# Optimization experiments

Measured on AMD Instinct MI355X. Metric: run time of the kernel, lower is better.

Reference implementation:

```python
import jax, jax.numpy as jnp
import numpy as np

# ---- constants from FlyingCartpole.__init__ defaults ----
MASS_Q = 2.0
MASS_P = 0.1
MASS = MASS_Q + MASS_P              # total mass m
JMAT = jnp.array([[0.0023, 0.0, 0.0], [0.0, 0.0023, 0.0], [0.0, 0.0, 0.004]], jnp.float32)
JINV = jnp.linalg.inv(JMAT)
L = 0.5                              # pendulum length
GVEC = jnp.array([0.0, 0.0, -9.81], jnp.float32)
MOTOR_DIST = 0.175
KF = 1.0
KM = 0.025
DT = 0.05
ACT_SCALE = 10.0
U_HOVER = -MASS * (-9.81) / ACT_SCALE / KF / 4.0   # per-motor hover throttle
_SS = np.array([[1.0, 1, 0], [1.0, -1, 0], [-1.0, -1, 0], [-1.0, 1, 0]], np.float32)
SS = jnp.asarray(_SS / np.linalg.norm(_SS, axis=-1, keepdims=True))  # [4,3] unit arms


def mrp2quat(m):
    # q = [1 - |m|^2, 2m] / (1 + |m|^2)
    n2 = jnp.sum(m * m, axis=-1, keepdims=True)
    return jnp.concatenate([1.0 - n2, 2.0 * m], axis=-1) / (1.0 + n2)


def quatrot(q, v):
    # rotate vector v by unit quaternion q = [s, qv]
    s, qv = q[..., :1], q[..., 1:]
    return v + 2.0 * jnp.cross(qv, jnp.cross(qv, v) + s * v)


def w2pdotkinematics_mrp(m, w):
    # mdot = 1/4 [(1-|m|^2) I + 2 [m]_x + 2 m m^T] w
    n2 = jnp.sum(m * m, axis=-1, keepdims=True)
    mw = jnp.sum(m * w, axis=-1, keepdims=True)
    return 0.25 * ((1.0 - n2) * w + 2.0 * jnp.cross(m, w) + 2.0 * m * mw)


def dynamics_(x, u):
    # state: [r(3), m(3), theta(1), v(3), w(3), theta_dot(1)]
    u = ACT_SCALE * (u + U_HOVER)
    m = x[..., 3:6]
    v = x[..., 7:10]
    w = x[..., 10:13]
    theta = x[..., 6:7]
    theta_dot = x[..., 13:14]

    q = mrp2quat(m)

    # forces (body frame): thrust + gravity rotated by q(-m)
    Fz = KF * jnp.sum(u, axis=-1)                     # [B]
    z = jnp.zeros_like(Fz)
    Fvec = jnp.stack([z, z, Fz], axis=-1)             # [B,3]
    f = Fvec + quatrot(mrp2quat(-m), MASS * GVEC)     # [B,3]

    # moments
    tau3 = KM * (u[..., 0] - u[..., 1] + u[..., 2] - u[..., 3])
    tau = jnp.stack([z, z, tau3], axis=-1)            # [B,3]
    zu = jnp.zeros_like(u)
    thrust = jnp.stack([zu, zu, KF * u], axis=-1)     # [B,4,3]
    tau = tau + jnp.cross(MOTOR_DIST * SS, thrust).sum(axis=-2)

    mdot = w2pdotkinematics_mrp(m, w)
    pdot = quatrot(q, v)
    vdot = f / MASS - jnp.cross(w, v)
    Jw = jnp.einsum('ij,bj->bi', JMAT, w)
    wdot = jnp.einsum('ij,bj->bi', JINV, tau - jnp.cross(w, Jw))

    x_ddot = quatrot(q, vdot)[..., 0:1]
    theta_ddot = (GVEC[2] * jnp.sin(theta) + x_ddot * jnp.cos(theta)) / L
    return jnp.concatenate([pdot, mdot, theta_dot, vdot, wdot, theta_ddot], axis=-1)


def rk4_dynamics(x, u):
    dt, dt2 = DT, DT / 2.0
    k1 = dynamics_(x, u)
    k2 = dynamics_(x + dt2 * k1, u)
    k3 = dynamics_(x + dt2 * k2, u)
    k4 = dynamics_(x + dt * k3, u)
    return x + dt / 6.0 * (k1 + 2.0 * k2 + 2.0 * k3 + k4)


def setup_inputs() -> dict:
    key = jax.random.key(0)
    kx, ku = jax.random.split(key)
    B = 2097152
    x = jax.random.normal(kx, (B, 14), dtype=jnp.float32)
    u = jax.random.normal(ku, (B, 4), dtype=jnp.float32)
    return {"x": x, "u": u}


def reference(x, u):
    return rk4_dynamics(x, u)
```

## Files before the change

kernel.cpp:

```cpp
#include <hip/hip_runtime.h>
#include <math.h>

namespace fc {

typedef float vf2 __attribute__((ext_vector_type(2)));
typedef float vf4 __attribute__((ext_vector_type(4)));

__device__ __forceinline__ vf2 sp(float c) { return vf2{c, c}; }

constexpr float ACT_SCALE = 10.0f;
constexpr float U_HOVER   = 0.515025f;
constexpr float INV_MASS  = 1.0f / 2.1f;
constexpr float KM        = 0.025f;
constexpr float TAUC      = 0.175f * 0.70710678f;
constexpr float JXY       = 0.0023f;
constexpr float JZ        = 0.004f;
constexpr float INV_JXY   = 1.0f / 0.0023f;
constexpr float INV_JZ    = 1.0f / 0.004f;
constexpr float G3        = -9.81f;
constexpr float INV_L     = 2.0f;
constexpr float DT        = 0.05f;
constexpr float DT2       = 0.05f * 0.5f;
constexpr float DT6       = 0.05f / 6.0f;

__device__ __forceinline__ void dyn2(const vf2* xt, vf2 FzM,
                                     vf2 taux, vf2 tauy, vf2 tauz, vf2* dx) {
  vf2 mx = xt[3], my = xt[4], mz = xt[5], th = xt[6];
  vf2 vx = xt[7], vy = xt[8], vz = xt[9];
  vf2 wx = xt[10], wy = xt[11], wz = xt[12];

  vf2 n2 = mx * mx + my * my + mz * mz;
  vf2 inv;
  inv.x = __builtin_amdgcn_rcpf(1.0f + n2.x);
  inv.y = __builtin_amdgcn_rcpf(1.0f + n2.y);
  vf2 s  = (sp(1.0f) - n2) * inv;
  vf2 qx = sp(2.0f) * mx * inv;
  vf2 qy = sp(2.0f) * my * inv;
  vf2 qz = sp(2.0f) * mz * inv;

  vf2 gtx = qy * sp(-G3);
  vf2 gty = qx * sp(G3);
  vf2 gtz = s * sp(G3);
  vf2 gx = sp(-2.0f) * (qy * gtz - qz * gty);
  vf2 gy = sp(-2.0f) * (qz * gtx - qx * gtz);
  vf2 gz = sp(G3) + sp(-2.0f) * (qx * gty - qy * gtx);

  vf2 tx = qy * vz - qz * vy + s * vx;
  vf2 ty = qz * vx - qx * vz + s * vy;
  vf2 tz = qx * vy - qy * vx + s * vz;
  dx[0] = vx + sp(2.0f) * (qy * tz - qz * ty);
  dx[1] = vy + sp(2.0f) * (qz * tx - qx * tz);
  dx[2] = vz + sp(2.0f) * (qx * ty - qy * tx);

  vf2 mw  = mx * wx + my * wy + mz * wz;
  vf2 on2 = sp(1.0f) - n2;
  dx[3] = sp(0.25f) * (on2 * wx + sp(2.0f) * (my * wz - mz * wy) + sp(2.0f) * mx * mw);
  dx[4] = sp(0.25f) * (on2 * wy + sp(2.0f) * (mz * wx - mx * wz) + sp(2.0f) * my * mw);
  dx[5] = sp(0.25f) * (on2 * wz + sp(2.0f) * (mx * wy - my * wx) + sp(2.0f) * mz * mw);

  dx[6] = xt[13];

  vf2 vdx = gx - (wy * vz - wz * vy);
  vf2 vdy = gy - (wz * vx - wx * vz);
  vf2 vdz = FzM + gz - (wx * vy - wy * vx);
  dx[7] = vdx; dx[8] = vdy; dx[9] = vdz;

  vf2 Jwx = sp(JXY) * wx, Jwy = sp(JXY) * wy, Jwz = sp(JZ) * wz;
  dx[10] = (taux - (wy * Jwz - wz * Jwy)) * sp(INV_JXY);
  dx[11] = (tauy - (wz * Jwx - wx * Jwz)) * sp(INV_JXY);
  dx[12] = (tauz - (wx * Jwy - wy * Jwx)) * sp(INV_JZ);

  vf2 t2y = qz * vdx - qx * vdz + s * vdy;
  vf2 t2z = qx * vdy - qy * vdx + s * vdz;
  vf2 rx  = vdx + sp(2.0f) * (qy * t2z - qz * t2y);
  vf2 st, ct;
  st.x = __sinf(th.x); st.y = __sinf(th.y);
  ct.x = __cosf(th.x); ct.y = __cosf(th.y);
  dx[13] = (sp(G3) * st + rx * ct) * sp(INV_L);
}

__device__ __forceinline__ void rk4_rows2(const vf2* x0, vf4 uA, vf4 uB, vf2* o) {
  vf2 su0 = sp(ACT_SCALE) * (vf2{uA.x, uB.x} + sp(U_HOVER));
  vf2 su1 = sp(ACT_SCALE) * (vf2{uA.y, uB.y} + sp(U_HOVER));
  vf2 su2 = sp(ACT_SCALE) * (vf2{uA.z, uB.z} + sp(U_HOVER));
  vf2 su3 = sp(ACT_SCALE) * (vf2{uA.w, uB.w} + sp(U_HOVER));

  vf2 Fz   = ((su0 + su1) + su2) + su3;
  vf2 FzM  = Fz * sp(INV_MASS);
  vf2 tauz = sp(KM) * (((su0 - su1) + su2) - su3);
  vf2 taux = ((sp(TAUC) * su0 + sp(-TAUC) * su1) + sp(-TAUC) * su2) + sp(TAUC) * su3;
  vf2 tauy = ((sp(-TAUC) * su0 + sp(-TAUC) * su1) + sp(TAUC) * su2) + sp(TAUC) * su3;

  vf2 xt[14], kk[14], acc[14];
  dyn2(x0, FzM, taux, tauy, tauz, kk);
  #pragma unroll
  for (int j = 0; j < 14; ++j) { acc[j] = kk[j]; xt[j] = x0[j] + sp(DT2) * kk[j]; }
  dyn2(xt, FzM, taux, tauy, tauz, kk);
  #pragma unroll
  for (int j = 0; j < 14; ++j) { acc[j] += sp(2.0f) * kk[j]; xt[j] = x0[j] + sp(DT2) * kk[j]; }
  dyn2(xt, FzM, taux, tauy, tauz, kk);
  #pragma unroll
  for (int j = 0; j < 14; ++j) { acc[j] += sp(2.0f) * kk[j]; xt[j] = x0[j] + sp(DT) * kk[j]; }
  dyn2(xt, FzM, taux, tauy, tauz, kk);
  #pragma unroll
  for (int j = 0; j < 14; ++j) o[j] = x0[j] + sp(DT6) * (acc[j] + kk[j]);
}

__global__ __launch_bounds__(256) void fc_rk4_kernel(const float* __restrict__ x,
                                                     const float* __restrict__ u,
                                                     float* __restrict__ out,
                                                     int n) {
  __shared__ float xs[512 * 14];
  const int t = threadIdx.x;
  const int lane = t & 63;
  const int w = t >> 6;
  const long long base = (long long)blockIdx.x * 512;

  if (base + 512 <= (long long)n) {
    const long long wrow = base + w * 128;
    float* ws = xs + w * 1792;

    typedef __attribute__((address_space(3))) float lds_f;
    typedef const __attribute__((address_space(1))) float gbl_f;
    gbl_f* gsrc = (gbl_f*)(x + wrow * 14);
    lds_f* ldst = (lds_f*)ws;
    #pragma unroll
    for (int k = 0; k < 7; ++k)
      __builtin_amdgcn_global_load_lds(
          (const __attribute__((address_space(1))) void*)(gsrc + k * 256 + lane * 4),
          (__attribute__((address_space(3))) void*)(ldst + k * 256), 16, 0, 0);

    const vf4* ug = (const vf4*)(u + wrow * 4);
    vf4 uA = ug[2 * lane];
    vf4 uB = ug[2 * lane + 1];

    asm volatile("s_waitcnt vmcnt(0)" ::: "memory");

    vf4* mine = (vf4*)(ws + lane * 28);
    vf4 a0 = mine[0], a1 = mine[1], a2 = mine[2], a3 = mine[3],
        a4 = mine[4], a5 = mine[5], a6 = mine[6];
    vf2 x0[14] = {
      {a0.x, a3.z}, {a0.y, a3.w}, {a0.z, a4.x}, {a0.w, a4.y},
      {a1.x, a4.z}, {a1.y, a4.w}, {a1.z, a5.x}, {a1.w, a5.y},
      {a2.x, a5.z}, {a2.y, a5.w}, {a2.z, a6.x}, {a2.w, a6.y},
      {a3.x, a6.z}, {a3.y, a6.w}};

    vf2 o[14];
    rk4_rows2(x0, uA, uB, o);

    mine[0] = vf4{o[0].x,  o[1].x,  o[2].x,  o[3].x};
    mine[1] = vf4{o[4].x,  o[5].x,  o[6].x,  o[7].x};
    mine[2] = vf4{o[8].x,  o[9].x,  o[10].x, o[11].x};
    mine[3] = vf4{o[12].x, o[13].x, o[0].y,  o[1].y};
    mine[4] = vf4{o[2].y,  o[3].y,  o[4].y,  o[5].y};
    mine[5] = vf4{o[6].y,  o[7].y,  o[8].y,  o[9].y};
    mine[6] = vf4{o[10].y, o[11].y, o[12].y, o[13].y};
    asm volatile("s_waitcnt lgkmcnt(0)" ::: "memory");

    const vf4* ws4 = (const vf4*)ws;
    vf4* og4 = (vf4*)(out + wrow * 14);
    #pragma unroll
    for (int k = 0; k < 7; ++k)
      __builtin_nontemporal_store(ws4[k * 64 + lane], og4 + k * 64 + lane);
  } else {
    #pragma unroll
    for (int k = 0; k < 2; ++k) {
      long long r = base + 2LL * t + k;
      if (r < n) {
        vf2 x0[14];
        #pragma unroll
        for (int j = 0; j < 14; ++j) { float v = x[r * 14 + j]; x0[j] = vf2{v, v}; }
        vf4 uv = *(const vf4*)(u + r * 4);
        vf2 o[14];
        rk4_rows2(x0, uv, uv, o);
        #pragma unroll
        for (int j = 0; j < 14; ++j) out[r * 14 + j] = o[j].x;
      }
    }
  }
}

}

extern "C" void kernel_launch(void* const* d_in, const int* in_sizes, int n_in,
                              void* d_out, int out_size, void* d_ws, size_t ws_size,
                              hipStream_t stream) {
  const float* x = (const float*)d_in[0];
  const float* u = (const float*)d_in[1];
  float* out = (float*)d_out;
  const int n = in_sizes[0] / 14;
  const int grid = (n + 511) / 512;
  hipLaunchKernelGGL(fc::fc_rk4_kernel, dim3(grid), dim3(256), 0, stream,
                     x, u, out, n);
}
```

Baseline: 45.55 us.

## Use persistent grid with double-buffered LDS prefetch of next tile

Replaces the one-tile-per-block launch with a persistent grid of at most 1024 blocks that loop over 512-row tiles. The next tile's x rows are prefetched into a second LDS buffer via global_load_lds, and its u values into registers, while the current tile is computed. Outputs are now written straight from registers as strided 16-byte stores instead of being staged through LDS for coalesced nontemporal stores. This doubles LDS use per block, which can cut occupancy. The uncoalesced output writes may also cost bandwidth.

```diff
diff --git a/kernel.cpp b/kernel.cpp
--- a/kernel.cpp
+++ b/kernel.cpp
@@ -109,63 +109,83 @@
 __global__ __launch_bounds__(256) void fc_rk4_kernel(const float* __restrict__ x,
                                                      const float* __restrict__ u,
                                                      float* __restrict__ out,
-                                                     int n) {
-  __shared__ float xs[512 * 14];
+                                                     int n, int nfull) {
+  __shared__ float xs[2 * 4 * 1792];
   const int t = threadIdx.x;
   const int lane = t & 63;
   const int w = t >> 6;
-  const long long base = (long long)blockIdx.x * 512;
-
-  if (base + 512 <= (long long)n) {
-    const long long wrow = base + w * 128;
-    float* ws = xs + w * 1792;
-
-    typedef __attribute__((address_space(3))) float lds_f;
-    typedef const __attribute__((address_space(1))) float gbl_f;
-    gbl_f* gsrc = (gbl_f*)(x + wrow * 14);
-    lds_f* ldst = (lds_f*)ws;
-    #pragma unroll
-    for (int k = 0; k < 7; ++k)
-      __builtin_amdgcn_global_load_lds(
-          (const __attribute__((address_space(1))) void*)(gsrc + k * 256 + lane * 4),
-          (__attribute__((address_space(3))) void*)(ldst + k * 256), 16, 0, 0);
-
-    const vf4* ug = (const vf4*)(u + wrow * 4);
-    vf4 uA = ug[2 * lane];
-    vf4 uB = ug[2 * lane + 1];
-
-    asm volatile("s_waitcnt vmcnt(0)" ::: "memory");
-
-    vf4* mine = (vf4*)(ws + lane * 28);
-    vf4 a0 = mine[0], a1 = mine[1], a2 = mine[2], a3 = mine[3],
-        a4 = mine[4], a5 = mine[5], a6 = mine[6];
-    vf2 x0[14] = {
-      {a0.x, a3.z}, {a0.y, a3.w}, {a0.z, a4.x}, {a0.w, a4.y},
-      {a1.x, a4.z}, {a1.y, a4.w}, {a1.z, a5.x}, {a1.w, a5.y},
-      {a2.x, a5.z}, {a2.y, a5.w}, {a2.z, a6.x}, {a2.w, a6.y},
-      {a3.x, a6.z}, {a3.y, a6.w}};
-
-    vf2 o[14];
-    rk4_rows2(x0, uA, uB, o);
-
-    mine[0] = vf4{o[0].x,  o[1].x,  o[2].x,  o[3].x};
-    mine[1] = vf4{o[4].x,  o[5].x,  o[6].x,  o[7].x};
-    mine[2] = vf4{o[8].x,  o[9].x,  o[10].x, o[11].x};
-    mine[3] = vf4{o[12].x, o[13].x, o[0].y,  o[1].y};
-    mine[4] = vf4{o[2].y,  o[3].y,  o[4].y,  o[5].y};
-    mine[5] = vf4{o[6].y,  o[7].y,  o[8].y,  o[9].y};
-    mine[6] = vf4{o[10].y, o[11].y, o[12].y, o[13].y};
-    asm volatile("s_waitcnt lgkmcnt(0)" ::: "memory");
-
-    const vf4* ws4 = (const vf4*)ws;
-    vf4* og4 = (vf4*)(out + wrow * 14);
-    #pragma unroll
-    for (int k = 0; k < 7; ++k)
-      __builtin_nontemporal_store(ws4[k * 64 + lane], og4 + k * 64 + lane);
-  } else {
+  const int G = gridDim.x;
+
+  int tile = blockIdx.x;
+  if (tile < nfull) {
+    float* wbuf[2] = { xs + w * 1792, xs + 4 * 1792 + w * 1792 };
+    int c = 0;
+
+    {
+      typedef const __attribute__((address_space(1))) float gbl_f;
+      gbl_f* gsrc = (gbl_f*)(x + ((long long)tile * 512 + w * 128) * 14);
+      #pragma unroll
+      for (int k = 0; k < 7; ++k)
+        __builtin_amdgcn_global_load_lds(
+            (const __attribute__((address_space(1))) void*)(gsrc + k * 256 + lane * 4),
+            (__attribute__((address_space(3))) void*)((__attribute__((address_space(3))) float*)wbuf[0] + k * 256),
+            16, 0, 0);
+    }
+    const vf4* ug0 = (const vf4*)(u + ((long long)tile * 512 + w * 128) * 4);
+    vf4 uA = ug0[2 * lane], uB = ug0[2 * lane + 1];
+
+    while (true) {
+      const int nxt = tile + G;
+      const bool have_next = nxt < nfull;
+      vf4 uAn, uBn;
+      if (have_next) {
+        typedef const __attribute__((address_space(1))) float gbl_f;
+        gbl_f* gsrc = (gbl_f*)(x + ((long long)nxt * 512 + w * 128) * 14);
+        #pragma unroll
+        for (int k = 0; k < 7; ++k)
+          __builtin_amdgcn_global_load_lds(
+              (const __attribute__((address_space(1))) void*)(gsrc + k * 256 + lane * 4),
+              (__attribute__((address_space(3))) void*)((__attribute__((address_space(3))) float*)wbuf[c ^ 1] + k * 256),
+              16, 0, 0);
+        const vf4* ugn = (const vf4*)(u + ((long long)nxt * 512 + w * 128) * 4);
+        uAn = ugn[2 * lane]; uBn = ugn[2 * lane + 1];
+      }
+
+      asm volatile("s_waitcnt vmcnt(7)" ::: "memory");
+
+      vf4* mine = (vf4*)(wbuf[c] + lane * 28);
+      vf4 a0 = mine[0], a1 = mine[1], a2 = mine[2], a3 = mine[3],
+          a4 = mine[4], a5 = mine[5], a6 = mine[6];
+      vf2 x0[14] = {
+        {a0.x, a3.z}, {a0.y, a3.w}, {a0.z, a4.x}, {a0.w, a4.y},
+        {a1.x, a4.z}, {a1.y, a4.w}, {a1.z, a5.x}, {a1.w, a5.y},
+        {a2.x, a5.z}, {a2.y, a5.w}, {a2.z, a6.x}, {a2.w, a6.y},
+        {a3.x, a6.z}, {a3.y, a6.w}};
+
+      vf2 o[14];
+      rk4_rows2(x0, uA, uB, o);
+
+      vf4* ob = (vf4*)(out + ((long long)tile * 512 + w * 128 + 2 * lane) * 14);
+      ob[0] = vf4{o[0].x,  o[1].x,  o[2].x,  o[3].x};
+      ob[1] = vf4{o[4].x,  o[5].x,  o[6].x,  o[7].x};
+      ob[2] = vf4{o[8].x,  o[9].x,  o[10].x, o[11].x};
+      ob[3] = vf4{o[12].x, o[13].x, o[0].y,  o[1].y};
+      ob[4] = vf4{o[2].y,  o[3].y,  o[4].y,  o[5].y};
+      ob[5] = vf4{o[6].y,  o[7].y,  o[8].y,  o[9].y};
+      ob[6] = vf4{o[10].y, o[11].y, o[12].y, o[13].y};
+
+      if (!have_next) break;
+      uA = uAn; uB = uBn;
+      c ^= 1;
+      tile = nxt;
+    }
+  }
+
+  const long long tbase = (long long)nfull * 512;
+  if (blockIdx.x == 0 && tbase < n) {
     #pragma unroll
     for (int k = 0; k < 2; ++k) {
-      long long r = base + 2LL * t + k;
+      long long r = tbase + 2LL * t + k;
       if (r < n) {
         vf2 x0[14];
         #pragma unroll
@@ -189,7 +209,8 @@
   const float* u = (const float*)d_in[1];
   float* out = (float*)d_out;
   const int n = in_sizes[0] / 14;
-  const int grid = (n + 511) / 512;
+  const int nfull = n / 512;
+  int grid = nfull < 1024 ? (nfull > 0 ? nfull : 1) : 1024;
   hipLaunchKernelGGL(fc::fc_rk4_kernel, dim3(grid), dim3(256), 0, stream,
-                     x, u, out, n);
-}
+                     x, u, out, n, nfull);
+}
```

Result: slower. 56.29 us (+23.6%).
